# Optimization experiments

Hardware: AMD Instinct MI355X
Metric: run time of the kernel (lower is better)

## Reference

```python
import jax, jax.numpy as jnp
import numpy as np
from jax import lax

SPARSITY = 0.5  # args.sparsity: fraction of weights KEPT


def get_subnet(scores, k):
    """GetSubnet.forward: sort |scores|, zero lowest (1-k) fraction, one elsewhere."""
    sa = jnp.abs(scores)
    n = sa.size
    j = int((1.0 - k) * n)  # static: number of entries zeroed
    idx = jnp.argsort(sa.ravel())  # ascending, matches torch .sort()
    mask = jnp.zeros((n,), dtype=sa.dtype).at[idx[j:]].set(1.0)
    return mask.reshape(scores.shape)


def masked_conv(x, w, s, b, stride):
    m = get_subnet(s, SPARSITY)
    y = lax.conv_general_dilated(
        x, w * m, window_strides=(stride, stride), padding=((1, 1), (1, 1)),
        dimension_numbers=('NCHW', 'OIHW', 'NCHW'))
    return y + b[None, :, None, None]


def setup_inputs() -> dict:
    key = jax.random.key(0)
    ks = jax.random.split(key, 16)
    def rn(k, shape, scale):
        return jax.random.normal(k, shape, dtype=jnp.float32) * scale
    return {
        'x':   rn(ks[0], (64, 3, 64, 64), 1.0),
        'w1':  rn(ks[1], (128, 3, 3, 3), 0.2),   's1': rn(ks[2], (128, 3, 3, 3), 1.0),   'b1': rn(ks[3], (128,), 0.01),
        'w2':  rn(ks[4], (256, 128, 3, 3), 0.05), 's2': rn(ks[5], (256, 128, 3, 3), 1.0), 'b2': rn(ks[6], (256,), 0.01),
        'w3':  rn(ks[7], (512, 256, 3, 3), 0.03), 's3': rn(ks[8], (512, 256, 3, 3), 1.0), 'b3': rn(ks[9], (512,), 0.01),
        'fw1': rn(ks[10], (1024, 512), 0.05),     'fs1': rn(ks[11], (1024, 512), 1.0),    'fb1': rn(ks[12], (1024,), 0.01),
        'fw2': rn(ks[13], (10, 1024), 0.05),      'fs2': rn(ks[14], (10, 1024), 1.0),     'fb2': rn(ks[15], (10,), 0.01),
    }


def reference(x, w1, s1, b1, w2, s2, b2, w3, s3, b3, fw1, fs1, fb1, fw2, fs2, fb2):
    h = jax.nn.relu(masked_conv(x, w1, s1, b1, stride=1))   # [64,128,64,64]
    h = jax.nn.relu(masked_conv(h, w2, s2, b2, stride=2))   # [64,256,32,32]
    h = jax.nn.relu(masked_conv(h, w3, s3, b3, stride=2))   # [64,512,16,16]
    h = h.mean(axis=(2, 3))                                 # [64,512] global avg pool
    m1 = get_subnet(fs1, SPARSITY)
    h = jax.nn.relu(h @ (fw1 * m1).T + fb1)                 # [64,1024]
    m2 = get_subnet(fs2, SPARSITY)
    return h @ (fw2 * m2).T + fb2                           # [64,10]
```

## Files before the change

kernel.cpp:

```cpp
#include <hip/hip_runtime.h>
#include <stdint.h>


typedef __attribute__((ext_vector_type(8))) short short8;
typedef __attribute__((ext_vector_type(4))) float floatx4;

__device__ __forceinline__ unsigned short f2bf(float f) {
    unsigned u = __float_as_uint(f);
    u += 0x7fffu + ((u >> 16) & 1u);
    return (unsigned short)(u >> 16);
}

constexpr unsigned CUM0 = 3456u;
constexpr unsigned CUM1 = 298368u;
constexpr unsigned CUM2 = 1478016u;
constexpr unsigned CUM3 = 2002304u;
constexpr unsigned STOT = 2012544u;
constexpr int NBH = 128;

__device__ __forceinline__ int find_tensor(unsigned idx, unsigned& li) {
    if (idx < CUM0) { li = idx;        return 0; }
    if (idx < CUM1) { li = idx - CUM0; return 1; }
    if (idx < CUM2) { li = idx - CUM1; return 2; }
    if (idx < CUM3) { li = idx - CUM2; return 3; }
    li = idx - CUM3; return 4;
}

__global__ __launch_bounds__(256) void hist8(const float* __restrict__ s0,
                                             const float* __restrict__ s1,
                                             const float* __restrict__ s2,
                                             const float* __restrict__ s3,
                                             const float* __restrict__ s4,
                                             const unsigned* __restrict__ P,
                                             unsigned* __restrict__ partials, int pass) {
    __shared__ unsigned lh[4 * 1280];
    const int tid = threadIdx.x;
    const int wv = tid >> 6;
    for (int i = tid; i < 4 * 1280; i += 256) lh[i] = 0;
    __syncthreads();

    const int hi_sh = 31 - 8 * pass;
    const int bin_sh = 23 - 8 * pass;
    unsigned pref[5];
    #pragma unroll
    for (int t = 0; t < 5; t++) pref[t] = pass ? P[t] : 0u;

    for (unsigned idx = blockIdx.x * 256u + tid; idx < STOT; idx += NBH * 256u) {
        unsigned li; int t = find_tensor(idx, li);
        const float* sp = t == 0 ? s0 : t == 1 ? s1 : t == 2 ? s2 : t == 3 ? s3 : s4;
        unsigned key = __float_as_uint(sp[li]) & 0x7fffffffu;
        if ((key >> hi_sh) == pref[t]) {
            unsigned bin = (pass == 3) ? (key & 127u) : ((key >> bin_sh) & 255u);
            atomicAdd(&lh[wv * 1280 + (unsigned)t * 256u + bin], 1u);
        }
    }
    __syncthreads();
    for (int i = tid; i < 1280; i += 256)
        partials[(size_t)blockIdx.x * 1280 + i] =
            lh[i] + lh[1280 + i] + lh[2560 + i] + lh[3840 + i];
}

__global__ __launch_bounds__(256) void find8(const unsigned* __restrict__ partials,
                                             unsigned* __restrict__ P,
                                             unsigned* __restrict__ targ, int pass) {
    const int t = blockIdx.x;
    const int tid = threadIdx.x;
    __shared__ unsigned bins[256];
    unsigned s = 0;
    for (int b = 0; b < NBH; b++) s += partials[(size_t)b * 1280 + t * 256 + tid];
    bins[tid] = s;
    __syncthreads();
    if (tid == 0) {
        unsigned n = t == 0 ? 3456u : t == 1 ? 294912u : t == 2 ? 1179648u
                   : t == 3 ? 524288u : 10240u;
        unsigned target = (pass == 0) ? (n >> 1) : targ[t];
        unsigned cum = 0; int b = 0;
        for (; b < 256; b++) { unsigned c = bins[b]; if (cum + c > target) break; cum += c; }
        targ[t] = target - cum;
        unsigned prev = (pass == 0) ? 0u : P[t];
        P[t] = (prev << ((pass == 3) ? 7 : 8)) | (unsigned)b;
    }
}

__global__ void mask_weights(const float* __restrict__ w0, const float* __restrict__ w1,
                             const float* __restrict__ w2, const float* __restrict__ w3,
                             const float* __restrict__ w4,
                             const float* __restrict__ s0, const float* __restrict__ s1,
                             const float* __restrict__ s2, const float* __restrict__ s3,
                             const float* __restrict__ s4,
                             const unsigned* __restrict__ T,
                             float* __restrict__ m0, float* __restrict__ m1,
                             float* __restrict__ m2, float* __restrict__ m3,
                             float* __restrict__ m4) {
    unsigned idx = blockIdx.x * 256u + threadIdx.x;
    if (idx >= STOT) return;
    unsigned li; int t = find_tensor(idx, li);
    const float* sp = t == 0 ? s0 : t == 1 ? s1 : t == 2 ? s2 : t == 3 ? s3 : s4;
    const float* wp = t == 0 ? w0 : t == 1 ? w1 : t == 2 ? w2 : t == 3 ? w3 : w4;
    float*       mp = t == 0 ? m0 : t == 1 ? m1 : t == 2 ? m2 : t == 3 ? m3 : m4;
    unsigned key = __float_as_uint(sp[li]) & 0x7fffffffu;
    mp[li] = (key >= T[t]) ? wp[li] : 0.f;
}

template <int KOUT, int CIN>
__global__ void reorder_w(const float* __restrict__ wm, unsigned short* __restrict__ A) {
    int t = blockIdx.x * 256 + threadIdx.x;
    if (t >= KOUT * CIN) return;
    int k = t / CIN, c = t % CIN;
    #pragma unroll
    for (int e = 0; e < 9; e++)
        A[((size_t)e * KOUT + k) * CIN + c] = f2bf(wm[(size_t)t * 9 + e]);
}

template <int C, int H, int W, int K, int TX, int TY, int KT>
__global__ __launch_bounds__(TX* TY) void conv_direct(const float* __restrict__ in,
                                                      const float* __restrict__ wm,
                                                      const float* __restrict__ bias,
                                                      unsigned short* __restrict__ out) {
    constexpr int TILW = TX * 2, TILH = TY * 2;
    constexpr int ITW = TILW + 2, ITH = TILH + 2;
    constexpr int NTHREADS = TX * TY;
    constexpr int NLOAD = (ITH * ITW + NTHREADS - 1) / NTHREADS;
    constexpr int KG = K / KT;

    __shared__ float sIn[ITH * ITW];
    __shared__ float sW[9 * KT];

    const int tid = threadIdx.x;
    const int tx = tid % TX, ty = tid / TX;
    const int kg = blockIdx.z % KG, n = blockIdx.z / KG;
    const int ox0 = blockIdx.x * TILW, oy0 = blockIdx.y * TILH;
    const int ix0 = ox0 - 1, iy0 = oy0 - 1;

    const float* inN = in + (size_t)n * C * H * W;
    const float* wkg = wm + (size_t)kg * KT * C * 9;

    int goff[NLOAD];
    #pragma unroll
    for (int i = 0; i < NLOAD; i++) {
        int idx = tid + i * NTHREADS;
        if (idx < ITH * ITW) {
            int r = idx / ITW, col = idx % ITW;
            int gy = iy0 + r, gx = ix0 + col;
            goff[i] = (gy >= 0 && gy < H && gx >= 0 && gx < W) ? (gy * W + gx) : -1;
        } else goff[i] = -2;
    }

    float acc[2][2][KT];
    #pragma unroll
    for (int py = 0; py < 2; py++)
        #pragma unroll
        for (int px = 0; px < 2; px++)
            #pragma unroll
            for (int j = 0; j < KT; j++) acc[py][px][j] = 0.f;

    for (int c = 0; c < C; c++) {
        const float* inC = inN + (size_t)c * H * W;
        #pragma unroll
        for (int i = 0; i < NLOAD; i++) {
            int g = goff[i];
            if (g >= -1) sIn[tid + i * NTHREADS] = (g >= 0) ? inC[g] : 0.f;
        }
        for (int i = tid; i < 9 * KT; i += NTHREADS) {
            int e = i / KT, j = i % KT;
            sW[i] = wkg[j * C * 9 + c * 9 + e];
        }
        __syncthreads();

        float vin[4][4];
        const float* base = &sIn[(ty * 2) * ITW + tx * 2];
        #pragma unroll
        for (int r = 0; r < 4; r++)
            #pragma unroll
            for (int cc = 0; cc < 4; cc++) vin[r][cc] = base[r * ITW + cc];

        #pragma unroll
        for (int e = 0; e < 9; e++) {
            const int dy = e / 3, dx = e % 3;
            #pragma unroll
            for (int j = 0; j < KT; j++) {
                float wv = sW[e * KT + j];
                #pragma unroll
                for (int py = 0; py < 2; py++)
                    #pragma unroll
                    for (int px = 0; px < 2; px++)
                        acc[py][px][j] = fmaf(vin[py + dy][px + dx], wv, acc[py][px][j]);
            }
        }
        __syncthreads();
    }

    #pragma unroll
    for (int j = 0; j < KT; j++) {
        float b = bias[kg * KT + j];
        #pragma unroll
        for (int py = 0; py < 2; py++)
            #pragma unroll
            for (int px = 0; px < 2; px++) {
                int oy = oy0 + ty * 2 + py, ox = ox0 + tx * 2 + px;
                float v = acc[py][px][j] + b;
                v = v > 0.f ? v : 0.f;
                out[(((size_t)n * K + kg * KT + j) * H + oy) * W + ox] = f2bf(v);
            }
    }
}

template <int C, int H, int W, int KOUT, int TOY, int TOX, bool POOL>
__global__ __launch_bounds__(256) void conv_mfma(const unsigned short* __restrict__ in,
                                                 const unsigned short* __restrict__ A,
                                                 const float* __restrict__ bias,
                                                 void* __restrict__ outv) {
    constexpr int OH = H / 2, OW = W / 2;
    constexpr int RH = 2 * TOY + 1, IW = 2 * TOX + 1;
    constexpr int HWv = H * W;
    constexpr int NC = C / 32;
    constexpr int NSLOT = RH * IW * 4;
    constexpr int SLMAX = (NSLOT + 255) / 256;

    __shared__ unsigned short sIn[RH * IW * 40];
    __shared__ unsigned short sWt[128 * 40];

    const int tid = threadIdx.x;
    const int lane = tid & 63;
    const int wv = tid >> 6;
    const int l15 = lane & 15;
    const int quad = lane >> 4;
    const int pt = blockIdx.x, kb = blockIdx.y, n = blockIdx.z;
    const int k0 = kb * 128;
    const int oy0 = pt * TOY;
    const int g0y = 2 * oy0 - 1;

    int soff[SLMAX], slds[SLMAX];
    #pragma unroll
    for (int i = 0; i < SLMAX; i++) {
        int s = tid + i * 256;
        if (s < NSLOT) {
            int ix = s % IW; int t2 = s / IW; int iy = t2 % RH; int c8 = t2 / RH;
            int gy = g0y + iy, gx = ix - 1;
            slds[i] = (iy * IW + ix) * 40 + c8 * 8;
            soff[i] = (gy >= 0 && gy < H && gx >= 0) ? (c8 * 8 * HWv + gy * W + gx) : -1;
        } else { soff[i] = -2; slds[i] = 0; }
    }

    int pB[8];
    #pragma unroll
    for (int fn = 0; fn < 8; fn++) {
        int p = fn * 16 + l15;
        int oyl = p / TOX, oxl = p % TOX;
        pB[fn] = (oyl * 2 * IW + oxl * 2) * 40 + quad * 8;
    }
    const int mw = wv * 32;

    floatx4 acc[2][8];
    #pragma unroll
    for (int fm = 0; fm < 2; fm++)
        #pragma unroll
        for (int fn = 0; fn < 8; fn++) acc[fm][fn] = (floatx4){0.f, 0.f, 0.f, 0.f};

    const int inN = n * C * HWv;

    for (int cc = 0; cc < NC; cc++) {
        __syncthreads();
        const int cbase = inN + cc * 32 * HWv;
        #pragma unroll
        for (int i = 0; i < SLMAX; i++) {
            int so = soff[i];
            if (so >= 0) {
                short8 v;
                #pragma unroll
                for (int j = 0; j < 8; j++) v[j] = (short)in[cbase + so + j * HWv];
                *(short8*)&sIn[slds[i]] = v;
            } else if (so == -1 && cc == 0) {
                *(short8*)&sIn[slds[i]] = (short8){0, 0, 0, 0, 0, 0, 0, 0};
            }
        }
        for (int e = 0; e < 9; e++) {
            __syncthreads();
            {
                const unsigned short* src = A + ((size_t)e * KOUT + k0) * C + cc * 32;
                #pragma unroll
                for (int i = 0; i < 2; i++) {
                    int s = tid + i * 256;
                    int k = s >> 2, c8 = s & 3;
                    short8 v = *(const short8*)(src + k * C + c8 * 8);
                    *(short8*)&sWt[k * 40 + c8 * 8] = v;
                }
            }
            __syncthreads();
            const int dy = e / 3, dx = e - dy * 3;
            const int boff = (dy * IW + dx) * 40;
            short8 afr[2], bfr[8];
            #pragma unroll
            for (int fm = 0; fm < 2; fm++)
                afr[fm] = *(const short8*)&sWt[(mw + fm * 16 + l15) * 40 + quad * 8];
            #pragma unroll
            for (int fn = 0; fn < 8; fn++)
                bfr[fn] = *(const short8*)&sIn[pB[fn] + boff];
            #pragma unroll
            for (int fm = 0; fm < 2; fm++)
                #pragma unroll
                for (int fn = 0; fn < 8; fn++)
                    acc[fm][fn] = __builtin_amdgcn_mfma_f32_16x16x32_bf16(
                        afr[fm], bfr[fn], acc[fm][fn], 0, 0, 0);
        }
    }

    if (!POOL) {
        unsigned short* out = (unsigned short*)outv;
        #pragma unroll
        for (int fm = 0; fm < 2; fm++) {
            #pragma unroll
            for (int reg = 0; reg < 4; reg++) {
                int k = k0 + mw + fm * 16 + quad * 4 + reg;
                float b = bias[k];
                #pragma unroll
                for (int fn = 0; fn < 8; fn++) {
                    int p = fn * 16 + l15;
                    int oy = oy0 + p / TOX, ox = p % TOX;
                    float v = acc[fm][fn][reg] + b;
                    v = v > 0.f ? v : 0.f;
                    out[((size_t)(n * KOUT + k) * OH + oy) * OW + ox] = f2bf(v);
                }
            }
        }
    } else {
        float* out = (float*)outv;
        #pragma unroll
        for (int fm = 0; fm < 2; fm++) {
            #pragma unroll
            for (int reg = 0; reg < 4; reg++) {
                int k = k0 + mw + fm * 16 + quad * 4 + reg;
                float b = bias[k];
                float s = 0.f;
                #pragma unroll
                for (int fn = 0; fn < 8; fn++) {
                    float v = acc[fm][fn][reg] + b;
                    s += v > 0.f ? v : 0.f;
                }
                s += __shfl_xor(s, 1); s += __shfl_xor(s, 2);
                s += __shfl_xor(s, 4); s += __shfl_xor(s, 8);
                if (l15 == 0) atomicAdd(&out[n * KOUT + k], s * (1.0f / (OH * OW)));
            }
        }
    }
}

__global__ void fc1_kernel(const float* __restrict__ pooled, const float* __restrict__ w,
                           const float* __restrict__ b, float* __restrict__ out) {
    int t = blockIdx.x * 256 + threadIdx.x;
    int o = t & 1023, n = t >> 10;
    const float4* w4 = (const float4*)(w + (size_t)o * 512);
    const float4* p4 = (const float4*)(pooled + (size_t)n * 512);
    float acc = 0.f;
    for (int i = 0; i < 128; i++) {
        float4 a = p4[i], ww = w4[i];
        acc += a.x * ww.x + a.y * ww.y + a.z * ww.z + a.w * ww.w;
    }
    acc += b[o];
    out[t] = acc > 0.f ? acc : 0.f;
}

__global__ void fc2_kernel(const float* __restrict__ h, const float* __restrict__ w,
                           const float* __restrict__ b, float* __restrict__ out) {
    int n = blockIdx.x, tid = threadIdx.x;
    __shared__ float redw[40];
    const float4* h4 = (const float4*)(h + (size_t)n * 1024);
    float4 a = h4[tid];
    for (int o = 0; o < 10; o++) {
        const float4* w4 = (const float4*)(w + (size_t)o * 1024);
        float4 ww = w4[tid];
        float v = a.x * ww.x + a.y * ww.y + a.z * ww.z + a.w * ww.w;
        for (int off = 32; off > 0; off >>= 1) v += __shfl_down(v, off);
        if ((tid & 63) == 0) redw[o * 4 + (tid >> 6)] = v;
    }
    __syncthreads();
    if (tid < 10) {
        float s = redw[tid * 4] + redw[tid * 4 + 1] + redw[tid * 4 + 2] + redw[tid * 4 + 3] + b[tid];
        out[n * 10 + tid] = s;
    }
}

extern "C" void kernel_launch(void* const* d_in, const int* in_sizes, int n_in,
                              void* d_out, int out_size, void* d_ws, size_t ws_size,
                              hipStream_t stream) {
    const float* x   = (const float*)d_in[0];
    const float* w1  = (const float*)d_in[1];
    const float* s1  = (const float*)d_in[2];
    const float* b1  = (const float*)d_in[3];
    const float* w2  = (const float*)d_in[4];
    const float* s2  = (const float*)d_in[5];
    const float* b2  = (const float*)d_in[6];
    const float* w3  = (const float*)d_in[7];
    const float* s3  = (const float*)d_in[8];
    const float* b3  = (const float*)d_in[9];
    const float* fw1 = (const float*)d_in[10];
    const float* fs1 = (const float*)d_in[11];
    const float* fb1 = (const float*)d_in[12];
    const float* fw2 = (const float*)d_in[13];
    const float* fs2 = (const float*)d_in[14];
    const float* fb2 = (const float*)d_in[15];
    float* out = (float*)d_out;

    char* ws = (char*)d_ws;
    size_t off = 0;
    auto alloc = [&](size_t bytes) -> char* {
        char* p = ws + off;
        off = (off + bytes + 255) & ~(size_t)255;
        return p;
    };
    unsigned* partials = (unsigned*)alloc((size_t)NBH * 1280 * 4);
    unsigned* P        = (unsigned*)alloc(64);
    unsigned* targ     = (unsigned*)alloc(64);
    float* wm1  = (float*)alloc(3456ull * 4);
    float* wm2  = (float*)alloc(294912ull * 4);
    float* wm3  = (float*)alloc(1179648ull * 4);
    float* fwm1 = (float*)alloc(524288ull * 4);
    float* fwm2 = (float*)alloc(10240ull * 4);
    unsigned short* A2 = (unsigned short*)alloc(294912ull * 2);
    unsigned short* A3 = (unsigned short*)alloc(1179648ull * 2);
    unsigned short* h1 = (unsigned short*)alloc(33554432ull * 2);
    unsigned short* h2 = (unsigned short*)alloc(16777216ull * 2);
    float* pooled = (float*)alloc(32768ull * 4);
    float* fc1h   = (float*)alloc(65536ull * 4);
    if (off > ws_size) return;

    (void)hipMemsetAsync(pooled, 0, 32768ull * 4, stream);

    for (int pass = 0; pass < 4; pass++) {
        hist8<<<NBH, 256, 0, stream>>>(s1, s2, s3, fs1, fs2, P, partials, pass);
        find8<<<5, 256, 0, stream>>>(partials, P, targ, pass);
    }
    int gs = (STOT + 255) / 256;
    mask_weights<<<gs, 256, 0, stream>>>(w1, w2, w3, fw1, fw2, s1, s2, s3, fs1, fs2, P,
                                         wm1, wm2, wm3, fwm1, fwm2);
    reorder_w<256, 128><<<128, 256, 0, stream>>>(wm2, A2);
    reorder_w<512, 256><<<512, 256, 0, stream>>>(wm3, A3);

    conv_direct<3, 64, 64, 128, 16, 16, 8>
        <<<dim3(2, 2, 64 * 16), 256, 0, stream>>>(x, wm1, b1, h1);
    conv_mfma<128, 64, 64, 256, 4, 32, false>
        <<<dim3(8, 2, 64), 256, 0, stream>>>(h1, A2, b2, h2);
    conv_mfma<256, 32, 32, 512, 8, 16, true>
        <<<dim3(2, 4, 64), 256, 0, stream>>>(h2, A3, b3, pooled);

    fc1_kernel<<<256, 256, 0, stream>>>(pooled, fwm1, fb1, fc1h);
    fc2_kernel<<<64, 256, 0, stream>>>(fc1h, fwm2, fb2, out);
}
```

Measured before the change: 467.1 us.

## Switch conv activations to NHWC and load MFMA fragments directly from global

Intermediate activations are now written in NHWC bf16, so the first conv stores 8 channels per vectorized write. The MFMA convolutions read A and B fragments straight from global memory as contiguous 8-channel vectors, with no LDS staging and no per-tap barriers, and use a 4x4 fragment tile per wave. The goal is to remove strided NCHW gathers and shared-memory synchronization. The mask and reorder kernels are also fused into one pass that writes bf16 reordered weights directly. The tradeoff is reliance on L1/L2 for reuse of overlapping input windows and weights, with more global load traffic.

```diff
diff --git a/kernel.cpp b/kernel.cpp
--- a/kernel.cpp
+++ b/kernel.cpp
@@ -3,6 +3,7 @@
 
 
 typedef __attribute__((ext_vector_type(8))) short short8;
+typedef __attribute__((ext_vector_type(4))) short short4v;
 typedef __attribute__((ext_vector_type(4))) float floatx4;
 
 __device__ __forceinline__ unsigned short f2bf(float f) {
@@ -82,34 +83,39 @@
     }
 }
 
-__global__ void mask_weights(const float* __restrict__ w0, const float* __restrict__ w1,
+__global__ void mask_reorder(const float* __restrict__ w0, const float* __restrict__ w1,
                              const float* __restrict__ w2, const float* __restrict__ w3,
                              const float* __restrict__ w4,
                              const float* __restrict__ s0, const float* __restrict__ s1,
                              const float* __restrict__ s2, const float* __restrict__ s3,
                              const float* __restrict__ s4,
                              const unsigned* __restrict__ T,
-                             float* __restrict__ m0, float* __restrict__ m1,
-                             float* __restrict__ m2, float* __restrict__ m3,
-                             float* __restrict__ m4) {
+                             float* __restrict__ wm1,
+                             unsigned short* __restrict__ A2,
+                             unsigned short* __restrict__ A3,
+                             float* __restrict__ fwm1, float* __restrict__ fwm2) {
     unsigned idx = blockIdx.x * 256u + threadIdx.x;
     if (idx >= STOT) return;
     unsigned li; int t = find_tensor(idx, li);
     const float* sp = t == 0 ? s0 : t == 1 ? s1 : t == 2 ? s2 : t == 3 ? s3 : s4;
     const float* wp = t == 0 ? w0 : t == 1 ? w1 : t == 2 ? w2 : t == 3 ? w3 : w4;
-    float*       mp = t == 0 ? m0 : t == 1 ? m1 : t == 2 ? m2 : t == 3 ? m3 : m4;
     unsigned key = __float_as_uint(sp[li]) & 0x7fffffffu;
-    mp[li] = (key >= T[t]) ? wp[li] : 0.f;
-}
-
-template <int KOUT, int CIN>
-__global__ void reorder_w(const float* __restrict__ wm, unsigned short* __restrict__ A) {
-    int t = blockIdx.x * 256 + threadIdx.x;
-    if (t >= KOUT * CIN) return;
-    int k = t / CIN, c = t % CIN;
-    #pragma unroll
-    for (int e = 0; e < 9; e++)
-        A[((size_t)e * KOUT + k) * CIN + c] = f2bf(wm[(size_t)t * 9 + e]);
+    float val = (key >= T[t]) ? wp[li] : 0.f;
+    if (t == 0) {
+        wm1[li] = val;
+    } else if (t == 1) {
+        unsigned k = li / 1152u, r = li - k * 1152u;
+        unsigned c = r / 9u, e = r - c * 9u;
+        A2[((size_t)e * 256u + k) * 128u + c] = f2bf(val);
+    } else if (t == 2) {
+        unsigned k = li / 2304u, r = li - k * 2304u;
+        unsigned c = r / 9u, e = r - c * 9u;
+        A3[((size_t)e * 512u + k) * 256u + c] = f2bf(val);
+    } else if (t == 3) {
+        fwm1[li] = val;
+    } else {
+        fwm2[li] = val;
+    }
 }
 
 template <int C, int H, int W, int K, int TX, int TY, int KT>
@@ -190,35 +196,32 @@
         __syncthreads();
     }
 
-    #pragma unroll
-    for (int j = 0; j < KT; j++) {
-        float b = bias[kg * KT + j];
-        #pragma unroll
-        for (int py = 0; py < 2; py++)
-            #pragma unroll
-            for (int px = 0; px < 2; px++) {
-                int oy = oy0 + ty * 2 + py, ox = ox0 + tx * 2 + px;
-                float v = acc[py][px][j] + b;
-                v = v > 0.f ? v : 0.f;
-                out[(((size_t)n * K + kg * KT + j) * H + oy) * W + ox] = f2bf(v);
+    float bj[KT];
+    #pragma unroll
+    for (int j = 0; j < KT; j++) bj[j] = bias[kg * KT + j];
+    #pragma unroll
+    for (int py = 0; py < 2; py++)
+        #pragma unroll
+        for (int px = 0; px < 2; px++) {
+            int oy = oy0 + ty * 2 + py, ox = ox0 + tx * 2 + px;
+            short8 v;
+            #pragma unroll
+            for (int j = 0; j < KT; j++) {
+                float t = acc[py][px][j] + bj[j];
+                v[j] = (short)f2bf(t > 0.f ? t : 0.f);
             }
-    }
-}
-
-template <int C, int H, int W, int KOUT, int TOY, int TOX, bool POOL>
-__global__ __launch_bounds__(256) void conv_mfma(const unsigned short* __restrict__ in,
-                                                 const unsigned short* __restrict__ A,
-                                                 const float* __restrict__ bias,
-                                                 void* __restrict__ outv) {
+            *(short8*)(out + ((size_t)(n * H + oy) * W + ox) * K + kg * KT) = v;
+        }
+}
+
+template <int C, int H, int W, int KOUT, bool POOL>
+__global__ __launch_bounds__(256, 3) void conv_nhwc(const unsigned short* __restrict__ in,
+                                                    const unsigned short* __restrict__ A,
+                                                    const float* __restrict__ bias,
+                                                    void* __restrict__ outv) {
     constexpr int OH = H / 2, OW = W / 2;
-    constexpr int RH = 2 * TOY + 1, IW = 2 * TOX + 1;
-    constexpr int HWv = H * W;
+    constexpr int PR = 128 / OW;
     constexpr int NC = C / 32;
-    constexpr int NSLOT = RH * IW * 4;
-    constexpr int SLMAX = (NSLOT + 255) / 256;
-
-    __shared__ unsigned short sIn[RH * IW * 40];
-    __shared__ unsigned short sWt[128 * 40];
 
     const int tid = threadIdx.x;
     const int lane = tid & 63;
@@ -226,80 +229,55 @@
     const int l15 = lane & 15;
     const int quad = lane >> 4;
     const int pt = blockIdx.x, kb = blockIdx.y, n = blockIdx.z;
-    const int k0 = kb * 128;
-    const int oy0 = pt * TOY;
-    const int g0y = 2 * oy0 - 1;
-
-    int soff[SLMAX], slds[SLMAX];
-    #pragma unroll
-    for (int i = 0; i < SLMAX; i++) {
-        int s = tid + i * 256;
-        if (s < NSLOT) {
-            int ix = s % IW; int t2 = s / IW; int iy = t2 % RH; int c8 = t2 / RH;
-            int gy = g0y + iy, gx = ix - 1;
-            slds[i] = (iy * IW + ix) * 40 + c8 * 8;
-            soff[i] = (gy >= 0 && gy < H && gx >= 0) ? (c8 * 8 * HWv + gy * W + gx) : -1;
-        } else { soff[i] = -2; slds[i] = 0; }
-    }
-
-    int pB[8];
-    #pragma unroll
-    for (int fn = 0; fn < 8; fn++) {
-        int p = fn * 16 + l15;
-        int oyl = p / TOX, oxl = p % TOX;
-        pB[fn] = (oyl * 2 * IW + oxl * 2) * 40 + quad * 8;
-    }
-    const int mw = wv * 32;
-
-    floatx4 acc[2][8];
-    #pragma unroll
-    for (int fm = 0; fm < 2; fm++)
-        #pragma unroll
-        for (int fn = 0; fn < 8; fn++) acc[fm][fn] = (floatx4){0.f, 0.f, 0.f, 0.f};
-
-    const int inN = n * C * HWv;
+    const int oy0 = pt * PR;
+    const int kw = (wv & 1) * 64;
+    const int pw = (wv >> 1) * 64;
+
+    int abase[4];
+    #pragma unroll
+    for (int fm = 0; fm < 4; fm++)
+        abase[fm] = (kb * 128 + kw + fm * 16 + l15) * C + quad * 8;
+
+    int pyb[4], xb[4];
+    #pragma unroll
+    for (int fn = 0; fn < 4; fn++) {
+        int p0 = pw + fn * 16;
+        int pr0 = p0 / OW, oxb = p0 % OW;
+        pyb[fn] = oy0 + pr0;
+        xb[fn] = 2 * (oxb + l15) - 1;
+    }
+
+    const unsigned short* inN = in + (size_t)n * H * W * C;
+
+    floatx4 acc[4][4];
+    #pragma unroll
+    for (int fm = 0; fm < 4; fm++)
+        #pragma unroll
+        for (int fn = 0; fn < 4; fn++) acc[fm][fn] = (floatx4){0.f, 0.f, 0.f, 0.f};
 
     for (int cc = 0; cc < NC; cc++) {
-        __syncthreads();
-        const int cbase = inN + cc * 32 * HWv;
-        #pragma unroll
-        for (int i = 0; i < SLMAX; i++) {
-            int so = soff[i];
-            if (so >= 0) {
-                short8 v;
+        const int cof = cc * 32 + quad * 8;
+        for (int e = 0; e < 9; e++) {
+            const int dy = e / 3, dx = e - dy * 3;
+            short8 afr[4], bfr[4];
+            #pragma unroll
+            for (int fm = 0; fm < 4; fm++)
+                afr[fm] = *(const short8*)(A + (size_t)e * KOUT * C + abase[fm] + cc * 32);
+            #pragma unroll
+            for (int fn = 0; fn < 4; fn++) {
+                int y = 2 * pyb[fn] + dy - 1;
+                short8 b = (short8){0, 0, 0, 0, 0, 0, 0, 0};
+                if (y >= 0 && y < H) {
+                    int x = xb[fn] + dx;
+                    if (x >= 0)
+                        b = *(const short8*)(inN + (y * W + x) * C + cof);
+                }
+                bfr[fn] = b;
+            }
+            #pragma unroll
+            for (int fm = 0; fm < 4; fm++)
                 #pragma unroll
-                for (int j = 0; j < 8; j++) v[j] = (short)in[cbase + so + j * HWv];
-                *(short8*)&sIn[slds[i]] = v;
-            } else if (so == -1 && cc == 0) {
-                *(short8*)&sIn[slds[i]] = (short8){0, 0, 0, 0, 0, 0, 0, 0};
-            }
-        }
-        for (int e = 0; e < 9; e++) {
-            __syncthreads();
-            {
-                const unsigned short* src = A + ((size_t)e * KOUT + k0) * C + cc * 32;
-                #pragma unroll
-                for (int i = 0; i < 2; i++) {
-                    int s = tid + i * 256;
-                    int k = s >> 2, c8 = s & 3;
-                    short8 v = *(const short8*)(src + k * C + c8 * 8);
-                    *(short8*)&sWt[k * 40 + c8 * 8] = v;
-                }
-            }
-            __syncthreads();
-            const int dy = e / 3, dx = e - dy * 3;
-            const int boff = (dy * IW + dx) * 40;
-            short8 afr[2], bfr[8];
-            #pragma unroll
-            for (int fm = 0; fm < 2; fm++)
-                afr[fm] = *(const short8*)&sWt[(mw + fm * 16 + l15) * 40 + quad * 8];
-            #pragma unroll
-            for (int fn = 0; fn < 8; fn++)
-                bfr[fn] = *(const short8*)&sIn[pB[fn] + boff];
-            #pragma unroll
-            for (int fm = 0; fm < 2; fm++)
-                #pragma unroll
-                for (int fn = 0; fn < 8; fn++)
+                for (int fn = 0; fn < 4; fn++)
                     acc[fm][fn] = __builtin_amdgcn_mfma_f32_16x16x32_bf16(
                         afr[fm], bfr[fn], acc[fm][fn], 0, 0, 0);
         }
@@ -308,33 +286,35 @@
     if (!POOL) {
         unsigned short* out = (unsigned short*)outv;
         #pragma unroll
-        for (int fm = 0; fm < 2; fm++) {
-            #pragma unroll
-            for (int reg = 0; reg < 4; reg++) {
-                int k = k0 + mw + fm * 16 + quad * 4 + reg;
-                float b = bias[k];
-                #pragma unroll
-                for (int fn = 0; fn < 8; fn++) {
-                    int p = fn * 16 + l15;
-                    int oy = oy0 + p / TOX, ox = p % TOX;
-                    float v = acc[fm][fn][reg] + b;
-                    v = v > 0.f ? v : 0.f;
-                    out[((size_t)(n * KOUT + k) * OH + oy) * OW + ox] = f2bf(v);
-                }
+        for (int fm = 0; fm < 4; fm++) {
+            const int k4 = kb * 128 + kw + fm * 16 + quad * 4;
+            float b0 = bias[k4], b1 = bias[k4 + 1], b2 = bias[k4 + 2], b3 = bias[k4 + 3];
+            #pragma unroll
+            for (int fn = 0; fn < 4; fn++) {
+                int oy = pyb[fn];
+                int ox = (xb[fn] + 1) >> 1;
+                float v0 = acc[fm][fn][0] + b0, v1 = acc[fm][fn][1] + b1;
+                float v2 = acc[fm][fn][2] + b2, v3 = acc[fm][fn][3] + b3;
+                short4v v;
+                v[0] = (short)f2bf(v0 > 0.f ? v0 : 0.f);
+                v[1] = (short)f2bf(v1 > 0.f ? v1 : 0.f);
+                v[2] = (short)f2bf(v2 > 0.f ? v2 : 0.f);
+                v[3] = (short)f2bf(v3 > 0.f ? v3 : 0.f);
+                *(short4v*)(out + ((size_t)(n * OH + oy) * OW + ox) * KOUT + k4) = v;
             }
         }
     } else {
         float* out = (float*)outv;
         #pragma unroll
-        for (int fm = 0; fm < 2; fm++) {
+        for (int fm = 0; fm < 4; fm++) {
             #pragma unroll
             for (int reg = 0; reg < 4; reg++) {
-                int k = k0 + mw + fm * 16 + quad * 4 + reg;
-                float b = bias[k];
+                int k = kb * 128 + kw + fm * 16 + quad * 4 + reg;
+                float bv = bias[k];
                 float s = 0.f;
                 #pragma unroll
-                for (int fn = 0; fn < 8; fn++) {
-                    float v = acc[fm][fn][reg] + b;
+                for (int fn = 0; fn < 4; fn++) {
+                    float v = acc[fm][fn][reg] + bv;
                     s += v > 0.f ? v : 0.f;
                 }
                 s += __shfl_xor(s, 1); s += __shfl_xor(s, 2);
@@ -412,8 +392,6 @@
     unsigned* P        = (unsigned*)alloc(64);
     unsigned* targ     = (unsigned*)alloc(64);
     float* wm1  = (float*)alloc(3456ull * 4);
-    float* wm2  = (float*)alloc(294912ull * 4);
-    float* wm3  = (float*)alloc(1179648ull * 4);
     float* fwm1 = (float*)alloc(524288ull * 4);
     float* fwm2 = (float*)alloc(10240ull * 4);
     unsigned short* A2 = (unsigned short*)alloc(294912ull * 2);
@@ -431,16 +409,14 @@
         find8<<<5, 256, 0, stream>>>(partials, P, targ, pass);
     }
     int gs = (STOT + 255) / 256;
-    mask_weights<<<gs, 256, 0, stream>>>(w1, w2, w3, fw1, fw2, s1, s2, s3, fs1, fs2, P,
-                                         wm1, wm2, wm3, fwm1, fwm2);
-    reorder_w<256, 128><<<128, 256, 0, stream>>>(wm2, A2);
-    reorder_w<512, 256><<<512, 256, 0, stream>>>(wm3, A3);
+    mask_reorder<<<gs, 256, 0, stream>>>(w1, w2, w3, fw1, fw2, s1, s2, s3, fs1, fs2, P,
+                                         wm1, A2, A3, fwm1, fwm2);
 
     conv_direct<3, 64, 64, 128, 16, 16, 8>
         <<<dim3(2, 2, 64 * 16), 256, 0, stream>>>(x, wm1, b1, h1);
-    conv_mfma<128, 64, 64, 256, 4, 32, false>
+    conv_nhwc<128, 64, 64, 256, false>
         <<<dim3(8, 2, 64), 256, 0, stream>>>(h1, A2, b2, h2);
-    conv_mfma<256, 32, 32, 512, 8, 16, true>
+    conv_nhwc<256, 32, 32, 512, true>
         <<<dim3(2, 4, 64), 256, 0, stream>>>(h2, A3, b3, pooled);
 
     fc1_kernel<<<256, 256, 0, stream>>>(pooled, fwm1, fb1, fc1h);
```

Result: slower. 610.3 us (+30.6%).
